# Kernel optimization log

Measured on AMD Instinct MI355X. Metric: run time of the kernel, lower is better.

## Reference

```python
import jax, jax.numpy as jnp
import numpy as np

D_MODEL = 1024
D_STATE = 16
D_CONV = 4
EXPAND = 2
D_INNER = EXPAND * D_MODEL          # 2048
DT_RANK = (D_MODEL + 15) // 16      # 64 (mamba 'auto')
B, L = 2, 1024


def _mamba_params(key, scale=0.02):
    ks = jax.random.split(key, 6)
    return dict(
        inW=jax.random.normal(ks[0], (2 * D_INNER, D_MODEL), jnp.float32) * scale,
        convW=jax.random.normal(ks[1], (D_INNER, 1, D_CONV), jnp.float32) * scale,
        convb=jnp.zeros((D_INNER,), jnp.float32),
        xprojW=jax.random.normal(ks[2], (DT_RANK + 2 * D_STATE, D_INNER), jnp.float32) * scale,
        dtW=jax.random.normal(ks[3], (D_INNER, DT_RANK), jnp.float32) * scale,
        dtb=jax.random.normal(ks[4], (D_INNER,), jnp.float32) * scale,
        A_log=jnp.log(jnp.tile(jnp.arange(1, D_STATE + 1, dtype=jnp.float32), (D_INNER, 1))),
        Dskip=jnp.ones((D_INNER,), jnp.float32),
        outW=jax.random.normal(ks[5], (D_MODEL, D_INNER), jnp.float32) * scale,
    )


def setup_inputs() -> dict:
    key = jax.random.key(0)
    kx, kf, kb, kp = jax.random.split(key, 4)
    inp = {"x": jax.random.normal(kx, (B, L, D_MODEL), jnp.float32)}
    inp["ln_w"] = jnp.ones((D_MODEL,), jnp.float32)
    inp["ln_b"] = jnp.zeros((D_MODEL,), jnp.float32)
    for pref, k in (("f_", kf), ("b_", kb)):
        for name, v in _mamba_params(k).items():
            inp[pref + name] = v
    inp["proj_W"] = jax.random.normal(kp, (D_MODEL, 2 * D_MODEL), jnp.float32) * 0.02
    inp["proj_b"] = jnp.zeros((D_MODEL,), jnp.float32)
    return inp


def _layernorm(x, w, b, eps=1e-5):
    mu = jnp.mean(x, axis=-1, keepdims=True)
    var = jnp.var(x, axis=-1, keepdims=True)
    return (x - mu) * jax.lax.rsqrt(var + eps) * w + b


def _mamba(x, inW, convW, convb, xprojW, dtW, dtb, A_log, Dskip, outW):
    # x: [B, L, d_model]
    xz = jnp.einsum('bld,ed->ble', x, inW)           # [B,L,2*d_inner]
    xs, z = jnp.split(xz, 2, axis=-1)                # each [B,L,d_inner]
    # depthwise causal conv over L
    xc = jnp.transpose(xs, (0, 2, 1))                # [B,d_inner,L]
    xc = jax.lax.conv_general_dilated(
        xc, convW, window_strides=(1,), padding=[(D_CONV - 1, 0)],
        feature_group_count=D_INNER)
    xs = jax.nn.silu(jnp.transpose(xc + convb[None, :, None], (0, 2, 1)))
    # input-dependent dt, B, C
    xdb = jnp.einsum('bld,ed->ble', xs, xprojW)      # [B,L,dt_rank+2*d_state]
    dt, Bm, Cm = jnp.split(xdb, [DT_RANK, DT_RANK + D_STATE], axis=-1)
    dt = jax.nn.softplus(jnp.einsum('blr,dr->bld', dt, dtW) + dtb)  # [B,L,d_inner]
    A = -jnp.exp(A_log)                              # [d_inner,d_state], negative
    dA = jnp.exp(dt[..., None] * A)                  # [B,L,d_inner,d_state]
    dBx = dt[..., None] * Bm[:, :, None, :] * xs[..., None]

    def step(h, inputs):
        dA_t, dBx_t, C_t = inputs                    # [B,d,s],[B,d,s],[B,s]
        h = h * dA_t + dBx_t
        y = jnp.einsum('bds,bs->bd', h, C_t)
        return h, y

    h0 = jnp.zeros((x.shape[0], D_INNER, D_STATE), x.dtype)
    _, ys = jax.lax.scan(step, h0, (jnp.moveaxis(dA, 1, 0),
                                    jnp.moveaxis(dBx, 1, 0),
                                    jnp.moveaxis(Cm, 1, 0)))
    y = jnp.moveaxis(ys, 0, 1)                       # [B,L,d_inner]
    y = (y + xs * Dskip) * jax.nn.silu(z)
    return jnp.einsum('bld,ed->ble', y, outW)        # [B,L,d_model]


def reference(x, ln_w, ln_b,
              f_inW, f_convW, f_convb, f_xprojW, f_dtW, f_dtb, f_A_log, f_Dskip, f_outW,
              b_inW, b_convW, b_convb, b_xprojW, b_dtW, b_dtb, b_A_log, b_Dskip, b_outW,
              proj_W, proj_b):
    normed = _layernorm(x, ln_w, ln_b)
    fwd_out = _mamba(normed, f_inW, f_convW, f_convb, f_xprojW, f_dtW, f_dtb,
                     f_A_log, f_Dskip, f_outW)
    bwd_out = _mamba(normed[:, ::-1, :], b_inW, b_convW, b_convb, b_xprojW, b_dtW,
                     b_dtb, b_A_log, b_Dskip, b_outW)[:, ::-1, :]
    combined = jnp.concatenate([fwd_out, bwd_out], axis=-1)
    return x + jnp.einsum('blc,ec->ble', combined, proj_W) + proj_b
```

## Files before the change

### kernel.cpp

```cpp
#include <hip/hip_runtime.h>
#include <hip/hip_bf16.h>
#include <math.h>

#define DM   1024
#define DI   2048
#define DTR  64
#define DST  16
#define NB   2
#define LL   1024
#define MR   (NB*LL)
#define XLD  128
#define KS   8

typedef __bf16 bf16x8 __attribute__((ext_vector_type(8)));
typedef float  f32x4  __attribute__((ext_vector_type(4)));

__device__ __forceinline__ float siluf(float x) { return x / (1.f + __expf(-x)); }
__device__ __forceinline__ float softplusf(float x) {
    return fmaxf(x, 0.f) + log1pf(__expf(-fabsf(x)));
}
__device__ __forceinline__ unsigned short f2bf(float f) {
    __hip_bfloat16 h = __float2bfloat16(f);
    return *reinterpret_cast<unsigned short*>(&h);
}
__device__ __forceinline__ float bf2f(__hip_bfloat16 h) { return __bfloat162float(h); }

__device__ __forceinline__ void gl2lds16(const __hip_bfloat16* g, __hip_bfloat16* l)
{
    __builtin_amdgcn_global_load_lds(
        (const __attribute__((address_space(1))) unsigned int*)g,
        (__attribute__((address_space(3))) unsigned int*)l, 16, 0, 0);
}

__global__ __launch_bounds__(256) void prep_k(
    const float* __restrict__ s0, const float* __restrict__ s1,
    const float* __restrict__ s2, const float* __restrict__ s3,
    const float* __restrict__ s4, __hip_bfloat16* __restrict__ warena,
    const float* __restrict__ fx, const float* __restrict__ bx,
    __hip_bfloat16* __restrict__ wpb2,
    const float* __restrict__ fo, const float* __restrict__ bo,
    __hip_bfloat16* __restrict__ wot,
    const float* __restrict__ x, const float* __restrict__ lnw,
    const float* __restrict__ lnb, __hip_bfloat16* __restrict__ nb)
{
    __shared__ float pshm[64 * 65];
    const int b = blockIdx.x;
    const int tid = threadIdx.x;

    if (b < 10496) {
        long idx = (long)b * 1024 + tid * 4;
        const float* src; long off;
        if      (idx <  4194304L) { src = s0; off = idx; }
        else if (idx <  8388608L) { src = s1; off = idx -  4194304L; }
        else if (idx < 10485760L) { src = s2; off = idx -  8388608L; }
        else if (idx < 10616832L) { src = s3; off = idx - 10485760L; }
        else                      { src = s4; off = idx - 10616832L; }
        float4 v = *(const float4*)(src + off);
        ushort4 o;
        o.x = f2bf(v.x); o.y = f2bf(v.y); o.z = f2bf(v.z); o.w = f2bf(v.w);
        *(ushort4*)((unsigned short*)warena + idx) = o;
    } else if (b < 10624) {
        int t = b - 10496;
        int z = t >> 6;
        const float* in = z ? bx : fx;
        int idx = ((t & 63) * 256 + tid) * 4;
        int row = idx >> 11;
        ushort4 o = make_ushort4(0, 0, 0, 0);
        if (row < 96) {
            float4 v = *(const float4*)(in + idx);
            o.x = f2bf(v.x); o.y = f2bf(v.y); o.z = f2bf(v.z); o.w = f2bf(v.w);
        }
        *(ushort4*)((unsigned short*)wpb2 + (size_t)z * 128 * DI + idx) = o;
    } else if (b < 11648) {
        int t = b - 10624;
        int z = t >> 9; t &= 511;
        const float* src = z ? bo : fo;
        int c0 = (t & 31) * 64;
        int r0 = (t >> 5) * 64;
        int tc = tid & 63;
        int tr = tid >> 6;
        #pragma unroll
        for (int ii = 0; ii < 16; ++ii) {
            int rl = tr + ii * 4;
            pshm[tc * 65 + rl] = src[(size_t)(r0 + rl) * DI + c0 + tc];
        }
        __syncthreads();
        __hip_bfloat16* dst = wot + (size_t)z * DI * DM;
        #pragma unroll
        for (int ii = 0; ii < 16; ++ii) {
            int cl = tr + ii * 4;
            dst[(size_t)(c0 + cl) * DM + r0 + tc] = __float2bfloat16(pshm[cl * 65 + tc]);
        }
    } else {
        int row = b - 11648;
        const float* xr = x + (size_t)row * DM;
        float4 v = *(const float4*)(xr + tid * 4);
        float s = v.x + v.y + v.z + v.w;
        float q = v.x*v.x + v.y*v.y + v.z*v.z + v.w*v.w;
        #pragma unroll
        for (int off = 32; off > 0; off >>= 1) {
            s += __shfl_xor(s, off, 64);
            q += __shfl_xor(q, off, 64);
        }
        int wv = tid >> 6;
        if ((tid & 63) == 0) { pshm[wv] = s; pshm[8 + wv] = q; }
        __syncthreads();
        s = pshm[0] + pshm[1] + pshm[2] + pshm[3];
        q = pshm[8] + pshm[9] + pshm[10] + pshm[11];
        float mu  = s * (1.f / DM);
        float var = q * (1.f / DM) - mu * mu;
        float rstd = rsqrtf(var + 1e-5f);
        float4 wv4 = *(const float4*)(lnw + tid * 4);
        float4 bv4 = *(const float4*)(lnb + tid * 4);
        ushort4 o;
        o.x = f2bf((v.x - mu) * rstd * wv4.x + bv4.x);
        o.y = f2bf((v.y - mu) * rstd * wv4.y + bv4.y);
        o.z = f2bf((v.z - mu) * rstd * wv4.z + bv4.z);
        o.w = f2bf((v.w - mu) * rstd * wv4.w + bv4.w);
        *(ushort4*)((unsigned short*)nb + (size_t)row * DM + tid * 4) = o;
    }
}

__global__ __launch_bounds__(256) void inproj_wcat_k(
    const __hip_bfloat16* __restrict__ nb,  const __hip_bfloat16* __restrict__ wbi,
    __hip_bfloat16* __restrict__ xz2,
    const __hip_bfloat16* __restrict__ pwb, const __hip_bfloat16* __restrict__ wot,
    __hip_bfloat16* __restrict__ wcat)
{
    __shared__ __hip_bfloat16 smem[2 * 128 * 64];
    const int z  = blockIdx.z;
    const int bxv = blockIdx.x, byv = blockIdx.y;
    if (z >= 2 && (bxv >= 16 || byv >= 8)) return;

    const __hip_bfloat16* Az;
    const __hip_bfloat16* Bz;
    __hip_bfloat16* Cz;
    int lda;
    if (z < 2) {
        Az = nb;                                lda = DM;
        Bz = wbi + (size_t)z * 2 * DI * DM;
        Cz = xz2 + (size_t)z * MR * 2 * DI;
    } else {
        Az = pwb + (size_t)(z - 2) * DM;        lda = 2 * DM;
        Bz = wot + (size_t)(z - 2) * DI * DM;
        Cz = wcat + (size_t)(z - 2) * DI;
    }
    const int ldb = DM, ldc = 2 * DI, K = DM;

    __hip_bfloat16* As = smem;
    __hip_bfloat16* Bs = smem + 128 * 64;
    const int tid  = threadIdx.x;
    const int bm   = byv * 128;
    const int bn   = bxv * 128;
    const int wv   = tid >> 6;
    const int lane = tid & 63;
    const int wr   = (wv >> 1) * 64;
    const int wc   = (wv & 1) * 64;
    const int srow = wv * 32 + (lane >> 3);
    const int cg   = ((lane & 7) ^ (lane >> 3)) * 8;
    const int fr   = lane & 15;
    const int quad = lane >> 4;
    const int pc0  = (quad ^ (fr & 7)) * 8;
    const int pc1  = ((4 + quad) ^ (fr & 7)) * 8;

    f32x4 acc[4][4] = {};

    for (int k0 = 0; k0 < K; k0 += 64) {
        __syncthreads();
        #pragma unroll
        for (int i = 0; i < 4; ++i) {
            int r = srow + i * 8;
            gl2lds16(Az + (size_t)(bm + r) * lda + k0 + cg, As + wv * 2048 + i * 512);
            gl2lds16(Bz + (size_t)(bn + r) * ldb + k0 + cg, Bs + wv * 2048 + i * 512);
        }
        __syncthreads();
        #pragma unroll
        for (int kk = 0; kk < 2; ++kk) {
            const int pc = kk ? pc1 : pc0;
            bf16x8 af[4], bf_[4];
            #pragma unroll
            for (int i = 0; i < 4; ++i) {
                af[i]  = *(const bf16x8*)(As + (wr + i * 16 + fr) * 64 + pc);
                bf_[i] = *(const bf16x8*)(Bs + (wc + i * 16 + fr) * 64 + pc);
            }
            #pragma unroll
            for (int i = 0; i < 4; ++i)
                #pragma unroll
                for (int j = 0; j < 4; ++j)
                    acc[i][j] = __builtin_amdgcn_mfma_f32_16x16x32_bf16(
                        af[i], bf_[j], acc[i][j], 0, 0, 0);
        }
    }

    float* eps = (float*)smem;
    const int half = wv >> 1;
    const int lrow = tid >> 3;
    const int cseg = (tid & 7) * 16;
    const int gr_  = bm + (lrow >> 4) * 64 + (lrow & 15);
    #pragma unroll
    for (int i = 0; i < 4; ++i) {
        __syncthreads();
        #pragma unroll
        for (int j = 0; j < 4; ++j)
            #pragma unroll
            for (int r = 0; r < 4; ++r)
                eps[(half * 16 + quad * 4 + r) * 132 + wc + j * 16 + fr] = acc[i][j][r];
        __syncthreads();
        float vals[16];
        *(float4*)(vals +  0) = *(const float4*)(eps + lrow * 132 + cseg +  0);
        *(float4*)(vals +  4) = *(const float4*)(eps + lrow * 132 + cseg +  4);
        *(float4*)(vals +  8) = *(const float4*)(eps + lrow * 132 + cseg +  8);
        *(float4*)(vals + 12) = *(const float4*)(eps + lrow * 132 + cseg + 12);
        int gr = gr_ + i * 16;
        int gc = bn + cseg;
        unsigned short os[16];
        #pragma unroll
        for (int c = 0; c < 16; ++c) os[c] = f2bf(vals[c]);
        unsigned short* dst = (unsigned short*)Cz + (size_t)gr * ldc + gc;
        *(ushort4*)(dst +  0) = *(ushort4*)(os +  0);
        *(ushort4*)(dst +  4) = *(ushort4*)(os +  4);
        *(ushort4*)(dst +  8) = *(ushort4*)(os +  8);
        *(ushort4*)(dst + 12) = *(ushort4*)(os + 12);
    }
}

template<int EPI>
__global__ __launch_bounds__(256) void gemm_gl(
    const __hip_bfloat16* __restrict__ A, int lda, size_t aofs,
    const __hip_bfloat16* __restrict__ B, int ldb, size_t bofs,
    void* __restrict__ Cp, int ldc, size_t cofs, int K,
    const float* __restrict__ bias0, const float* __restrict__ bias1)
{
    __shared__ __hip_bfloat16 smem[2 * 128 * 64];
    __hip_bfloat16* As = smem;
    __hip_bfloat16* Bs = smem + 128 * 64;
    const int tid  = threadIdx.x;
    const int z    = blockIdx.z;
    const int bm   = blockIdx.y * 128;
    const int bn   = blockIdx.x * 128;
    const __hip_bfloat16* Az = A + (size_t)z * aofs;
    const __hip_bfloat16* Bz = B + (size_t)z * bofs;
    const int wv   = tid >> 6;
    const int lane = tid & 63;
    const int wr   = (wv >> 1) * 64;
    const int wc   = (wv & 1) * 64;
    const int srow = wv * 32 + (lane >> 3);
    const int cg   = ((lane & 7) ^ (lane >> 3)) * 8;
    const int fr   = lane & 15;
    const int quad = lane >> 4;
    const int pc0  = (quad ^ (fr & 7)) * 8;
    const int pc1  = ((4 + quad) ^ (fr & 7)) * 8;

    f32x4 acc[4][4] = {};

    for (int k0 = 0; k0 < K; k0 += 64) {
        __syncthreads();
        #pragma unroll
        for (int i = 0; i < 4; ++i) {
            int r = srow + i * 8;
            gl2lds16(Az + (size_t)(bm + r) * lda + k0 + cg, As + wv * 2048 + i * 512);
            gl2lds16(Bz + (size_t)(bn + r) * ldb + k0 + cg, Bs + wv * 2048 + i * 512);
        }
        __syncthreads();
        #pragma unroll
        for (int kk = 0; kk < 2; ++kk) {
            const int pc = kk ? pc1 : pc0;
            bf16x8 af[4], bf_[4];
            #pragma unroll
            for (int i = 0; i < 4; ++i) {
                af[i]  = *(const bf16x8*)(As + (wr + i * 16 + fr) * 64 + pc);
                bf_[i] = *(const bf16x8*)(Bs + (wc + i * 16 + fr) * 64 + pc);
            }
            #pragma unroll
            for (int i = 0; i < 4; ++i)
                #pragma unroll
                for (int j = 0; j < 4; ++j)
                    acc[i][j] = __builtin_amdgcn_mfma_f32_16x16x32_bf16(
                        af[i], bf_[j], acc[i][j], 0, 0, 0);
        }
    }

    const float* bias = (EPI == 3) ? (z ? bias1 : bias0) : nullptr;
    float* eps = (float*)smem;
    const int half = wv >> 1;
    const int lrow = tid >> 3;
    const int cseg = (tid & 7) * 16;
    const int gr_  = bm + (lrow >> 4) * 64 + (lrow & 15);
    #pragma unroll
    for (int i = 0; i < 4; ++i) {
        __syncthreads();
        #pragma unroll
        for (int j = 0; j < 4; ++j)
            #pragma unroll
            for (int r = 0; r < 4; ++r)
                eps[(half * 16 + quad * 4 + r) * 132 + wc + j * 16 + fr] = acc[i][j][r];
        __syncthreads();
        float vals[16];
        *(float4*)(vals +  0) = *(const float4*)(eps + lrow * 132 + cseg +  0);
        *(float4*)(vals +  4) = *(const float4*)(eps + lrow * 132 + cseg +  4);
        *(float4*)(vals +  8) = *(const float4*)(eps + lrow * 132 + cseg +  8);
        *(float4*)(vals + 12) = *(const float4*)(eps + lrow * 132 + cseg + 12);
        int gr = gr_ + i * 16;
        int gc = bn + cseg;
        if (EPI == 0) {
            float* dst = (float*)Cp + (size_t)z * cofs + (size_t)gr * ldc + gc;
            *(float4*)(dst +  0) = *(const float4*)(vals +  0);
            *(float4*)(dst +  4) = *(const float4*)(vals +  4);
            *(float4*)(dst +  8) = *(const float4*)(vals +  8);
            *(float4*)(dst + 12) = *(const float4*)(vals + 12);
        } else {
            unsigned short os[16];
            #pragma unroll
            for (int c = 0; c < 16; ++c) {
                float t = vals[c];
                if (EPI == 3) t = softplusf(t + bias[gc + c]);
                os[c] = f2bf(t);
            }
            unsigned short* dst = (unsigned short*)Cp + (size_t)z * cofs +
                                  (size_t)gr * ldc + gc;
            *(ushort4*)(dst +  0) = *(ushort4*)(os +  0);
            *(ushort4*)(dst +  4) = *(ushort4*)(os +  4);
            *(ushort4*)(dst +  8) = *(ushort4*)(os +  8);
            *(ushort4*)(dst + 12) = *(ushort4*)(os + 12);
        }
    }
}

__global__ __launch_bounds__(256) void xproj_part_k(
    const __hip_bfloat16* __restrict__ A,
    const __hip_bfloat16* __restrict__ B,
    float* __restrict__ part)
{
    __shared__ __hip_bfloat16 smem[2 * 128 * 64];
    __hip_bfloat16* As = smem;
    __hip_bfloat16* Bs = smem + 128 * 64;
    const int tid  = threadIdx.x;
    const int ks   = blockIdx.x;
    const int bm   = blockIdx.y * 128;
    const int z    = blockIdx.z;
    const __hip_bfloat16* Az = A + (size_t)z * MR * DI;
    const __hip_bfloat16* Bz = B + (size_t)z * 128 * DI;
    const int kb   = ks * (DI / KS);
    const int wv   = tid >> 6;
    const int lane = tid & 63;
    const int wr   = (wv >> 1) * 64;
    const int wc   = (wv & 1) * 64;
    const int srow = wv * 32 + (lane >> 3);
    const int cg   = ((lane & 7) ^ (lane >> 3)) * 8;
    const int fr   = lane & 15;
    const int quad = lane >> 4;
    const int pc0  = (quad ^ (fr & 7)) * 8;
    const int pc1  = ((4 + quad) ^ (fr & 7)) * 8;

    f32x4 acc[4][4] = {};

    #pragma unroll
    for (int k0 = 0; k0 < DI / KS; k0 += 64) {
        __syncthreads();
        #pragma unroll
        for (int i = 0; i < 4; ++i) {
            int r = srow + i * 8;
            gl2lds16(Az + (size_t)(bm + r) * DI + kb + k0 + cg, As + wv * 2048 + i * 512);
            gl2lds16(Bz + (size_t)r * DI + kb + k0 + cg,        Bs + wv * 2048 + i * 512);
        }
        __syncthreads();
        #pragma unroll
        for (int kk = 0; kk < 2; ++kk) {
            const int pc = kk ? pc1 : pc0;
            bf16x8 af[4], bf_[4];
            #pragma unroll
            for (int i = 0; i < 4; ++i) {
                af[i]  = *(const bf16x8*)(As + (wr + i * 16 + fr) * 64 + pc);
                bf_[i] = *(const bf16x8*)(Bs + (wc + i * 16 + fr) * 64 + pc);
            }
            #pragma unroll
            for (int i = 0; i < 4; ++i)
                #pragma unroll
                for (int j = 0; j < 4; ++j)
                    acc[i][j] = __builtin_amdgcn_mfma_f32_16x16x32_bf16(
                        af[i], bf_[j], acc[i][j], 0, 0, 0);
        }
    }

    float* dst = part + ((size_t)z * KS + ks) * MR * XLD;
    const int er = quad * 4;
    #pragma unroll
    for (int i = 0; i < 4; ++i)
        #pragma unroll
        for (int j = 0; j < 4; ++j) {
            int row = bm + wr + i * 16 + er;
            int col = wc + j * 16 + fr;
            #pragma unroll
            for (int r = 0; r < 4; ++r)
                dst[(size_t)(row + r) * XLD + col] = acc[i][j][r];
        }
}

__global__ __launch_bounds__(256) void xproj_reduce_k(
    const float* __restrict__ part, float* __restrict__ xdb,
    __hip_bfloat16* __restrict__ xdbt)
{
    int z = blockIdx.y;
    size_t idx = ((size_t)blockIdx.x * 256 + threadIdx.x) * 4;
    const float* p = part + (size_t)z * KS * MR * XLD;
    float4 s = make_float4(0.f, 0.f, 0.f, 0.f);
    #pragma unroll
    for (int ks = 0; ks < KS; ++ks) {
        float4 v = *(const float4*)(p + (size_t)ks * MR * XLD + idx);
        s.x += v.x; s.y += v.y; s.z += v.z; s.w += v.w;
    }
    *(float4*)(xdb + (size_t)z * MR * XLD + idx) = s;
    int c = (int)(idx & (XLD - 1));
    if (c < 64) {
        size_t m = idx >> 7;
        ushort4 o;
        o.x = f2bf(s.x); o.y = f2bf(s.y); o.z = f2bf(s.z); o.w = f2bf(s.w);
        *(ushort4*)((unsigned short*)xdbt + (size_t)z * MR * 64 + m * 64 + c) = o;
    }
}

__global__ __launch_bounds__(256) void conv_silu_k(
    const __hip_bfloat16* __restrict__ xz2,
    const float* __restrict__ fW, const float* __restrict__ fb,
    const float* __restrict__ bW, const float* __restrict__ bb_,
    __hip_bfloat16* __restrict__ xsb2)
{
    int dirv = blockIdx.y;
    int idx = blockIdx.x * 256 + threadIdx.x;
    int d = idx & (DI - 1);
    int m = idx >> 11;
    int t = m & (LL - 1);
    int bb = m >> 10;
    const float* w  = (dirv ? bW : fW) + d * 4;
    const __hip_bfloat16* xz = xz2 + (size_t)dirv * MR * 2 * DI;
    float acc = (dirv ? bb_ : fb)[d];
    if (dirv == 0) {
        #pragma unroll
        for (int k = 0; k < 4; ++k) {
            int tt = t - 3 + k;
            if (tt >= 0)
                acc = fmaf(w[k], bf2f(xz[(size_t)(bb * LL + tt) * (2 * DI) + d]), acc);
        }
    } else {
        #pragma unroll
        for (int k = 0; k < 4; ++k) {
            int tt = t + 3 - k;
            if (tt < LL)
                acc = fmaf(w[k], bf2f(xz[(size_t)(bb * LL + tt) * (2 * DI) + d]), acc);
        }
    }
    xsb2[(size_t)dirv * MR * DI + (size_t)m * DI + d] = __float2bfloat16(siluf(acc));
}

__global__ __launch_bounds__(256) void scan1_k(
    const __hip_bfloat16* __restrict__ dtf2, const __hip_bfloat16* __restrict__ xsb2,
    const float* __restrict__ xdb2,
    const float* __restrict__ fA, const float* __restrict__ bA,
    float* __restrict__ hend, float* __restrict__ aprod, int G, int Cn)
{
    int d  = blockIdx.x * 256 + threadIdx.x;
    int bb = blockIdx.y;
    int zz = blockIdx.z;
    int dirv = (zz >= G) ? 1 : 0;
    int g = zz - (dirv ? G : 0);
    const float* A_log = dirv ? bA : fA;
    const __hip_bfloat16* dtf = dtf2 + (size_t)dirv * MR * DI;
    const __hip_bfloat16* xs = xsb2 + (size_t)dirv * MR * DI;
    const float* xdb = xdb2 + (size_t)dirv * MR * XLD;
    size_t hoff = (size_t)dirv * G * (NB * DI * DST);

    float Ad[DST], h[DST], ap[DST];
    bool pw = true;
    #pragma unroll
    for (int s = 0; s < DST; ++s) {
        Ad[s] = -__expf(A_log[d * DST + s]);
        pw = pw && (fabsf(Ad[s] + (float)(s + 1)) < 1e-3f * (s + 1));
        h[s] = 0.f; ap[s] = 1.f;
    }
    int i0 = g * Cn;
    for (int i = 0; i < Cn; ++i) {
        int ii = i0 + i;
        int t = dirv ? (LL - 1 - ii) : ii;
        size_t m = (size_t)bb * LL + t;
        float dtv = bf2f(dtf[m * DI + d]);
        float xv  = bf2f(xs[m * DI + d]);
        const float* bc = xdb + m * XLD;
        float dtx = dtv * xv;
        float dAv[DST];
        if (pw) {
            float r = __expf(-dtv);
            float a = r;
            #pragma unroll
            for (int s = 0; s < DST; ++s) { dAv[s] = a; a *= r; }
        } else {
            #pragma unroll
            for (int s = 0; s < DST; ++s) dAv[s] = __expf(dtv * Ad[s]);
        }
        #pragma unroll
        for (int s = 0; s < DST; ++s) {
            h[s] = fmaf(h[s], dAv[s], dtx * bc[64 + s]);
            ap[s] *= dAv[s];
        }
    }
    size_t base = hoff + ((size_t)(g * NB + bb) * DI + d) * DST;
    #pragma unroll
    for (int s = 0; s < DST; s += 4) {
        *(float4*)(hend  + base + s) = make_float4(h[s], h[s+1], h[s+2], h[s+3]);
        *(float4*)(aprod + base + s) = make_float4(ap[s], ap[s+1], ap[s+2], ap[s+3]);
    }
}

__global__ __launch_bounds__(256) void scan2_k(
    float* __restrict__ hend, const float* __restrict__ aprod, int G)
{
    int dirv = blockIdx.y;
    int idx = blockIdx.x * 256 + threadIdx.x;
    const int slab = NB * DI * DST;
    size_t hoff = (size_t)dirv * G * slab;
    float carry = 0.f;
    for (int g = 0; g < G; ++g) {
        size_t off = hoff + (size_t)g * slab + idx;
        float a = aprod[off];
        float e = hend[off];
        hend[off] = carry;
        carry = fmaf(a, carry, e);
    }
}

__global__ __launch_bounds__(256) void scan3_k(
    const __hip_bfloat16* __restrict__ dtf2, const __hip_bfloat16* __restrict__ xsb2,
    const float* __restrict__ xdb2, const __hip_bfloat16* __restrict__ xz2,
    const float* __restrict__ fA, const float* __restrict__ bA,
    const float* __restrict__ fD, const float* __restrict__ bD,
    const float* __restrict__ hin, __hip_bfloat16* __restrict__ ycat, int G, int Cn)
{
    int d  = blockIdx.x * 256 + threadIdx.x;
    int bb = blockIdx.y;
    int zz = blockIdx.z;
    int dirv = (zz >= G) ? 1 : 0;
    int g = zz - (dirv ? G : 0);
    const float* A_log = dirv ? bA : fA;
    const float* Dskip = dirv ? bD : fD;
    const __hip_bfloat16* dtf = dtf2 + (size_t)dirv * MR * DI;
    const __hip_bfloat16* xs = xsb2 + (size_t)dirv * MR * DI;
    const float* xdb = xdb2 + (size_t)dirv * MR * XLD;
    const __hip_bfloat16* xz = xz2 + (size_t)dirv * MR * 2 * DI;
    size_t hoff = (size_t)dirv * G * (NB * DI * DST);

    float Ad[DST], h[DST];
    bool pw = true;
    size_t base = hoff + ((size_t)(g * NB + bb) * DI + d) * DST;
    #pragma unroll
    for (int s = 0; s < DST; ++s) {
        Ad[s] = -__expf(A_log[d * DST + s]);
        pw = pw && (fabsf(Ad[s] + (float)(s + 1)) < 1e-3f * (s + 1));
        h[s] = hin[base + s];
    }
    float Dsk = Dskip[d];
    int i0 = g * Cn;
    for (int i = 0; i < Cn; ++i) {
        int ii = i0 + i;
        int t = dirv ? (LL - 1 - ii) : ii;
        size_t m = (size_t)bb * LL + t;
        float dtv = bf2f(dtf[m * DI + d]);
        float xv  = bf2f(xs[m * DI + d]);
        const float* bc = xdb + m * XLD;
        float dtx = dtv * xv;
        float dAv[DST];
        if (pw) {
            float r = __expf(-dtv);
            float a = r;
            #pragma unroll
            for (int s = 0; s < DST; ++s) { dAv[s] = a; a *= r; }
        } else {
            #pragma unroll
            for (int s = 0; s < DST; ++s) dAv[s] = __expf(dtv * Ad[s]);
        }
        float yv = 0.f;
        #pragma unroll
        for (int s = 0; s < DST; ++s) {
            h[s] = fmaf(h[s], dAv[s], dtx * bc[64 + s]);
            yv = fmaf(h[s], bc[80 + s], yv);
        }
        float zv = bf2f(xz[m * (2 * DI) + DI + d]);
        ycat[m * (2 * DI) + (size_t)dirv * DI + d] =
            __float2bfloat16((yv + xv * Dsk) * siluf(zv));
    }
}

__global__ __launch_bounds__(256) void scan_mono_k(
    const __hip_bfloat16* __restrict__ dtf2, const __hip_bfloat16* __restrict__ xsb2,
    const float* __restrict__ xdb2, const __hip_bfloat16* __restrict__ xz2,
    const float* __restrict__ fA, const float* __restrict__ bA,
    const float* __restrict__ fD, const float* __restrict__ bD,
    __hip_bfloat16* __restrict__ ycat)
{
    int d  = blockIdx.x * 256 + threadIdx.x;
    int bb = blockIdx.y;
    int dirv = blockIdx.z;
    const float* A_log = dirv ? bA : fA;
    const float* Dskip = dirv ? bD : fD;
    const __hip_bfloat16* dtf = dtf2 + (size_t)dirv * MR * DI;
    const __hip_bfloat16* xs = xsb2 + (size_t)dirv * MR * DI;
    const float* xdb = xdb2 + (size_t)dirv * MR * XLD;
    const __hip_bfloat16* xz = xz2 + (size_t)dirv * MR * 2 * DI;
    float Ad[DST], h[DST];
    #pragma unroll
    for (int s = 0; s < DST; ++s) { Ad[s] = -__expf(A_log[d * DST + s]); h[s] = 0.f; }
    float Dsk = Dskip[d];
    for (int i = 0; i < LL; ++i) {
        int t = dirv ? (LL - 1 - i) : i;
        size_t m = (size_t)bb * LL + t;
        float dtv = bf2f(dtf[m * DI + d]);
        float xv  = bf2f(xs[m * DI + d]);
        const float* bc = xdb + m * XLD;
        float dtx = dtv * xv;
        float yv = 0.f;
        #pragma unroll
        for (int s = 0; s < DST; ++s) {
            float dA = __expf(dtv * Ad[s]);
            h[s] = fmaf(h[s], dA, dtx * bc[64 + s]);
            yv = fmaf(h[s], bc[80 + s], yv);
        }
        float zv = bf2f(xz[m * (2 * DI) + DI + d]);
        ycat[m * (2 * DI) + (size_t)dirv * DI + d] =
            __float2bfloat16((yv + xv * Dsk) * siluf(zv));
    }
}

__global__ __launch_bounds__(256) void final_reduce_k(
    const float* __restrict__ part, const float* __restrict__ x,
    const float* __restrict__ proj_b, float* __restrict__ out)
{
    size_t idx = ((size_t)blockIdx.x * 256 + threadIdx.x) * 4;
    float4 s = make_float4(0.f, 0.f, 0.f, 0.f);
    #pragma unroll
    for (int z = 0; z < 4; ++z) {
        float4 v = *(const float4*)(part + (size_t)z * MR * DM + idx);
        s.x += v.x; s.y += v.y; s.z += v.z; s.w += v.w;
    }
    float4 xv = *(const float4*)(x + idx);
    float4 pb = *(const float4*)(proj_b + (idx & (DM - 1)));
    float4 o;
    o.x = xv.x + pb.x + s.x;
    o.y = xv.y + pb.y + s.y;
    o.z = xv.z + pb.z + s.z;
    o.w = xv.w + pb.w + s.w;
    *(float4*)(out + idx) = o;
}

extern "C" void kernel_launch(void* const* d_in, const int* in_sizes, int n_in,
                              void* d_out, int out_size, void* d_ws, size_t ws_size,
                              hipStream_t stream)
{
    const float* x      = (const float*)d_in[0];
    const float* ln_w   = (const float*)d_in[1];
    const float* ln_b   = (const float*)d_in[2];
    const float* f_inW    = (const float*)d_in[3];
    const float* f_convW  = (const float*)d_in[4];
    const float* f_convb  = (const float*)d_in[5];
    const float* f_xprojW = (const float*)d_in[6];
    const float* f_dtW    = (const float*)d_in[7];
    const float* f_dtb    = (const float*)d_in[8];
    const float* f_A_log  = (const float*)d_in[9];
    const float* f_Dskip  = (const float*)d_in[10];
    const float* f_outW   = (const float*)d_in[11];
    const float* b_inW    = (const float*)d_in[12];
    const float* b_convW  = (const float*)d_in[13];
    const float* b_convb  = (const float*)d_in[14];
    const float* b_xprojW = (const float*)d_in[15];
    const float* b_dtW    = (const float*)d_in[16];
    const float* b_dtb    = (const float*)d_in[17];
    const float* b_A_log  = (const float*)d_in[18];
    const float* b_Dskip  = (const float*)d_in[19];
    const float* b_outW   = (const float*)d_in[20];
    const float* proj_W = (const float*)d_in[21];
    const float* proj_b = (const float*)d_in[22];

    float* ws = (float*)d_ws;
    size_t o = 0;
    __hip_bfloat16* xz2  = (__hip_bfloat16*)(ws + o);
    float* fpart = ws + o;
    o += (size_t)2 * MR * 2 * DI / 2;
    __hip_bfloat16* xsb2 = (__hip_bfloat16*)(ws + o); o += (size_t)2 * MR * DI / 2;
    __hip_bfloat16* ycat = (__hip_bfloat16*)(ws + o);
    float* xpart = ws + o;
    o += (size_t)MR * 2 * DI / 2;
    float* xdb2 = ws + o; o += (size_t)2 * MR * XLD;
    __hip_bfloat16* xdbt = (__hip_bfloat16*)(ws + o); o += (size_t)2 * MR * 64 / 2;
    __hip_bfloat16* dtfb = (__hip_bfloat16*)(ws + o); o += (size_t)2 * MR * DI / 2;
    __hip_bfloat16* nb = (__hip_bfloat16*)(ws + o); o += (size_t)MR * DM / 2;
    __hip_bfloat16* warena = (__hip_bfloat16*)(ws + o); o += 15466496 / 2;
    float* hbuf = ws + o;
    size_t base_floats = o;

    __hip_bfloat16* wbi  = warena;
    __hip_bfloat16* pwb  = warena +  8388608;
    __hip_bfloat16* wdt  = warena + 10485760;
    __hip_bfloat16* wpb2 = warena + 10747904;
    __hip_bfloat16* wcat = warena + 11272192;

    const size_t slab = (size_t)NB * DI * DST;
    int G = 32;
    while (G > 4 && (base_floats + 4ull * G * slab) * 4 > ws_size) G >>= 1;
    int useChunks = ((base_floats + 4ull * G * slab) * 4 <= ws_size);
    float* hend  = hbuf;
    float* aprod = hbuf + 2ull * G * slab;
    int Cn = useChunks ? LL / G : LL;

    int wotInHbuf = useChunks && (4ull * G * slab >= 2097152ull);
    __hip_bfloat16* wot = wotInHbuf ? (__hip_bfloat16*)hbuf : xz2;

    prep_k<<<13696, 256, 0, stream>>>(
        f_inW, b_inW, proj_W, f_dtW, b_dtW, warena,
        f_xprojW, b_xprojW, wpb2,
        f_outW, b_outW, wot,
        x, ln_w, ln_b, nb);

    if (wotInHbuf) {
        inproj_wcat_k<<<dim3(32, 16, 4), 256, 0, stream>>>(
            nb, wbi, xz2, pwb, wot, wcat);
    } else {
        gemm_gl<1><<<dim3(DI / 128, DM / 128, 2), 256, 0, stream>>>(
            pwb, 2 * DM, (size_t)DM, wot, DM, (size_t)DI * DM,
            wcat, 2 * DI, (size_t)DI, DM, nullptr, nullptr);
        inproj_wcat_k<<<dim3(32, 16, 2), 256, 0, stream>>>(
            nb, wbi, xz2, pwb, wot, wcat);
    }

    conv_silu_k<<<dim3((MR * DI) / 256, 2), 256, 0, stream>>>(
        xz2, f_convW, f_convb, b_convW, b_convb, xsb2);

    xproj_part_k<<<dim3(KS, MR / 128, 2), 256, 0, stream>>>(xsb2, wpb2, xpart);
    xproj_reduce_k<<<dim3((MR * XLD) / 1024, 2), 256, 0, stream>>>(xpart, xdb2, xdbt);

    gemm_gl<3><<<dim3(DI / 128, MR / 128, 2), 256, 0, stream>>>(
        xdbt, 64, (size_t)MR * 64, wdt, 64, (size_t)DI * 64,
        dtfb, DI, (size_t)MR * DI, 64, f_dtb, b_dtb);

    if (useChunks) {
        scan1_k<<<dim3(DI / 256, NB, 2 * G), 256, 0, stream>>>(
            dtfb, xsb2, xdb2, f_A_log, b_A_log, hend, aprod, G, Cn);
        scan2_k<<<dim3((NB * DI * DST) / 256, 2), 256, 0, stream>>>(hend, aprod, G);
        scan3_k<<<dim3(DI / 256, NB, 2 * G), 256, 0, stream>>>(
            dtfb, xsb2, xdb2, xz2, f_A_log, b_A_log, f_Dskip, b_Dskip,
            hend, ycat, G, Cn);
    } else {
        scan_mono_k<<<dim3(DI / 256, NB, 2), 256, 0, stream>>>(
            dtfb, xsb2, xdb2, xz2, f_A_log, b_A_log, f_Dskip, b_Dskip, ycat);
    }

    gemm_gl<0><<<dim3(DM / 128, MR / 128, 4), 256, 0, stream>>>(
        ycat, 2 * DI, 1024, wcat, 2 * DI, 1024,
        fpart, DM, (size_t)MR * DM, 1024, nullptr, nullptr);

    final_reduce_k<<<(MR * DM) / 1024, 256, 0, stream>>>(
        fpart, x, proj_b, (float*)d_out);
}
```

Baseline: 423.2 us.

## Replace in-projection GEMM with 256x256-tile, 4-stage pipelined 512-thread kernel

The combined in-projection/wcat kernel is replaced by a dedicated in-projection GEMM that uses 256x256 output tiles with 512 threads. It streams K in 32-wide slices through a 4-deep LDS ring with explicit vmcnt waits, split barriers and MFMA priority hints. Blocks are remapped so the two directions interleave across the grid. The wcat product moves back to a separate gemm_gl launch. The larger tile raises data reuse and hides load latency, but it launches only 256 blocks, uses 128 KB of LDS per block and adds a kernel launch.

```diff
diff --git a/kernel.cpp b/kernel.cpp
--- a/kernel.cpp
+++ b/kernel.cpp
@@ -121,106 +121,117 @@
     }
 }
 
-__global__ __launch_bounds__(256) void inproj_wcat_k(
-    const __hip_bfloat16* __restrict__ nb,  const __hip_bfloat16* __restrict__ wbi,
-    __hip_bfloat16* __restrict__ xz2,
-    const __hip_bfloat16* __restrict__ pwb, const __hip_bfloat16* __restrict__ wot,
-    __hip_bfloat16* __restrict__ wcat)
-{
-    __shared__ __hip_bfloat16 smem[2 * 128 * 64];
-    const int z  = blockIdx.z;
-    const int bxv = blockIdx.x, byv = blockIdx.y;
-    if (z >= 2 && (bxv >= 16 || byv >= 8)) return;
-
-    const __hip_bfloat16* Az;
-    const __hip_bfloat16* Bz;
-    __hip_bfloat16* Cz;
-    int lda;
-    if (z < 2) {
-        Az = nb;                                lda = DM;
-        Bz = wbi + (size_t)z * 2 * DI * DM;
-        Cz = xz2 + (size_t)z * MR * 2 * DI;
-    } else {
-        Az = pwb + (size_t)(z - 2) * DM;        lda = 2 * DM;
-        Bz = wot + (size_t)(z - 2) * DI * DM;
-        Cz = wcat + (size_t)(z - 2) * DI;
-    }
-    const int ldb = DM, ldc = 2 * DI, K = DM;
-
-    __hip_bfloat16* As = smem;
-    __hip_bfloat16* Bs = smem + 128 * 64;
-    const int tid  = threadIdx.x;
-    const int bm   = byv * 128;
-    const int bn   = bxv * 128;
+__global__ __launch_bounds__(512) void inproj256_k(
+    const __hip_bfloat16* __restrict__ A,
+    const __hip_bfloat16* __restrict__ Bmat,
+    __hip_bfloat16* __restrict__ C)
+{
+    __shared__ __hip_bfloat16 smem[65536];
+    const int tid = threadIdx.x;
+    int id = blockIdx.x;
+    int s  = (id & 7) * 32 + (id >> 3);
+    const int z  = s >> 7;
+    const int r  = s & 127;
+    const int bm = (r & 7) * 256;
+    const int bn = (r >> 3) * 256;
+    const __hip_bfloat16* Az = A;
+    const __hip_bfloat16* Bz = Bmat + (size_t)z * 2 * DI * DM;
+    __hip_bfloat16* Cz = C + (size_t)z * MR * 2 * DI;
+
     const int wv   = tid >> 6;
     const int lane = tid & 63;
-    const int wr   = (wv >> 1) * 64;
-    const int wc   = (wv & 1) * 64;
-    const int srow = wv * 32 + (lane >> 3);
-    const int cg   = ((lane & 7) ^ (lane >> 3)) * 8;
+    const int wm   = wv >> 2;
+    const int wn   = wv & 3;
     const int fr   = lane & 15;
     const int quad = lane >> 4;
-    const int pc0  = (quad ^ (fr & 7)) * 8;
-    const int pc1  = ((4 + quad) ^ (fr & 7)) * 8;
-
-    f32x4 acc[4][4] = {};
-
-    for (int k0 = 0; k0 < K; k0 += 64) {
-        __syncthreads();
-        #pragma unroll
-        for (int i = 0; i < 4; ++i) {
-            int r = srow + i * 8;
-            gl2lds16(Az + (size_t)(bm + r) * lda + k0 + cg, As + wv * 2048 + i * 512);
-            gl2lds16(Bz + (size_t)(bn + r) * ldb + k0 + cg, Bs + wv * 2048 + i * 512);
-        }
-        __syncthreads();
-        #pragma unroll
-        for (int kk = 0; kk < 2; ++kk) {
-            const int pc = kk ? pc1 : pc0;
-            bf16x8 af[4], bf_[4];
-            #pragma unroll
-            for (int i = 0; i < 4; ++i) {
-                af[i]  = *(const bf16x8*)(As + (wr + i * 16 + fr) * 64 + pc);
-                bf_[i] = *(const bf16x8*)(Bs + (wc + i * 16 + fr) * 64 + pc);
-            }
-            #pragma unroll
-            for (int i = 0; i < 4; ++i)
+
+    const int r0   = tid >> 2;
+    const int ksel = ((tid & 3) ^ ((r0 >> 1) & 3)) * 8;
+    const int kph  = (quad ^ ((fr >> 1) & 3)) * 8;
+    const int aoff = (wm * 128 + fr) * 32 + kph;
+    const int boff = (wn * 64  + fr) * 32 + kph;
+
+    __hip_bfloat16* const Asl = smem;
+    __hip_bfloat16* const Bsl = smem + 32768;
+
+    f32x4 acc[8][4] = {};
+
+#define STG_A(T) { int q_ = (T) & 3; \
+    _Pragma("unroll") for (int l = 0; l < 2; ++l) \
+        gl2lds16(Az + (size_t)(bm + l * 128 + r0) * DM + (T) * 32 + ksel, \
+                 Asl + q_ * 8192 + l * 4096 + wv * 512); }
+#define STG_B(T) { int q_ = (T) & 3; \
+    _Pragma("unroll") for (int l = 0; l < 2; ++l) \
+        gl2lds16(Bz + (size_t)(bn + l * 128 + r0) * DM + (T) * 32 + ksel, \
+                 Bsl + q_ * 8192 + l * 4096 + wv * 512); }
+
+    STG_A(0); STG_B(0); STG_A(1); STG_B(1); STG_A(2); STG_B(2);
+
+#define TILE(T, VM, DOST) { \
+    asm volatile("s_barrier" ::: "memory");                \
+    if (DOST) { STG_A((T) + 3); } \
+    asm volatile("s_waitcnt vmcnt(" #VM ")" ::: "memory"); \
+    asm volatile("s_barrier" ::: "memory");                \
+    const __hip_bfloat16* At = Asl + ((T) & 3) * 8192; \
+    const __hip_bfloat16* Bt = Bsl + ((T) & 3) * 8192; \
+    bf16x8 bfr[4], afr[4]; \
+    _Pragma("unroll") for (int j = 0; j < 4; ++j) \
+        bfr[j] = *(const bf16x8*)(Bt + boff + j * 512); \
+    _Pragma("unroll") for (int i = 0; i < 4; ++i) \
+        afr[i] = *(const bf16x8*)(At + aoff + i * 512); \
+    __builtin_amdgcn_s_setprio(1); \
+    _Pragma("unroll") for (int i = 0; i < 4; ++i) \
+        _Pragma("unroll") for (int j = 0; j < 4; ++j) \
+            acc[i][j] = __builtin_amdgcn_mfma_f32_16x16x32_bf16( \
+                afr[i], bfr[j], acc[i][j], 0, 0, 0); \
+    __builtin_amdgcn_s_setprio(0); \
+    if (DOST) { STG_B((T) + 3); } \
+    asm volatile("s_barrier" ::: "memory");                \
+    _Pragma("unroll") for (int i = 0; i < 4; ++i) \
+        afr[i] = *(const bf16x8*)(At + aoff + (4 + i) * 512); \
+    __builtin_amdgcn_s_setprio(1); \
+    _Pragma("unroll") for (int i = 0; i < 4; ++i) \
+        _Pragma("unroll") for (int j = 0; j < 4; ++j) \
+            acc[4 + i][j] = __builtin_amdgcn_mfma_f32_16x16x32_bf16( \
+                afr[i], bfr[j], acc[4 + i][j], 0, 0, 0); \
+    __builtin_amdgcn_s_setprio(0); \
+}
+
+    for (int t = 0; t < 29; ++t) { TILE(t, 10, 1); }
+    TILE(29, 8, 0);
+    TILE(30, 4, 0);
+    TILE(31, 0, 0);
+#undef TILE
+#undef STG_A
+#undef STG_B
+
+    float* eps = (float*)smem;
+    const int orow = tid >> 3;
+    const int ocol = (tid & 7) * 32;
+    #pragma unroll
+    for (int p = 0; p < 4; ++p) {
+        __syncthreads();
+        if (wm == (p >> 1)) {
+            int ib = (p & 1) * 4;
+            #pragma unroll
+            for (int i2 = 0; i2 < 4; ++i2)
                 #pragma unroll
                 for (int j = 0; j < 4; ++j)
-                    acc[i][j] = __builtin_amdgcn_mfma_f32_16x16x32_bf16(
-                        af[i], bf_[j], acc[i][j], 0, 0, 0);
-        }
-    }
-
-    float* eps = (float*)smem;
-    const int half = wv >> 1;
-    const int lrow = tid >> 3;
-    const int cseg = (tid & 7) * 16;
-    const int gr_  = bm + (lrow >> 4) * 64 + (lrow & 15);
-    #pragma unroll
-    for (int i = 0; i < 4; ++i) {
-        __syncthreads();
-        #pragma unroll
-        for (int j = 0; j < 4; ++j)
-            #pragma unroll
-            for (int r = 0; r < 4; ++r)
-                eps[(half * 16 + quad * 4 + r) * 132 + wc + j * 16 + fr] = acc[i][j][r];
-        __syncthreads();
-        float vals[16];
-        *(float4*)(vals +  0) = *(const float4*)(eps + lrow * 132 + cseg +  0);
-        *(float4*)(vals +  4) = *(const float4*)(eps + lrow * 132 + cseg +  4);
-        *(float4*)(vals +  8) = *(const float4*)(eps + lrow * 132 + cseg +  8);
-        *(float4*)(vals + 12) = *(const float4*)(eps + lrow * 132 + cseg + 12);
-        int gr = gr_ + i * 16;
-        int gc = bn + cseg;
-        unsigned short os[16];
-        #pragma unroll
-        for (int c = 0; c < 16; ++c) os[c] = f2bf(vals[c]);
-        unsigned short* dst = (unsigned short*)Cz + (size_t)gr * ldc + gc;
-        *(ushort4*)(dst +  0) = *(ushort4*)(os +  0);
-        *(ushort4*)(dst +  4) = *(ushort4*)(os +  4);
-        *(ushort4*)(dst +  8) = *(ushort4*)(os +  8);
-        *(ushort4*)(dst + 12) = *(ushort4*)(os + 12);
+                    #pragma unroll
+                    for (int rr = 0; rr < 4; ++rr)
+                        eps[(i2 * 16 + quad * 4 + rr) * 260 + wn * 64 + j * 16 + fr]
+                            = acc[ib + i2][j][rr];
+        }
+        __syncthreads();
+        unsigned short os[32] __attribute__((aligned(16)));
+        #pragma unroll
+        for (int c = 0; c < 32; ++c) os[c] = f2bf(eps[orow * 260 + ocol + c]);
+        unsigned short* dst = (unsigned short*)Cz +
+            (size_t)(bm + p * 64 + orow) * (2 * DI) + bn + ocol;
+        *(uint4*)(dst +  0) = *(const uint4*)(os +  0);
+        *(uint4*)(dst +  8) = *(const uint4*)(os +  8);
+        *(uint4*)(dst + 16) = *(const uint4*)(os + 16);
+        *(uint4*)(dst + 24) = *(const uint4*)(os + 24);
     }
 }
 
@@ -718,14 +729,15 @@
         x, ln_w, ln_b, nb);
 
     if (wotInHbuf) {
-        inproj_wcat_k<<<dim3(32, 16, 4), 256, 0, stream>>>(
-            nb, wbi, xz2, pwb, wot, wcat);
+        inproj256_k<<<256, 512, 0, stream>>>(nb, wbi, xz2);
+        gemm_gl<1><<<dim3(DI / 128, DM / 128, 2), 256, 0, stream>>>(
+            pwb, 2 * DM, (size_t)DM, wot, DM, (size_t)DI * DM,
+            wcat, 2 * DI, (size_t)DI, DM, nullptr, nullptr);
     } else {
         gemm_gl<1><<<dim3(DI / 128, DM / 128, 2), 256, 0, stream>>>(
             pwb, 2 * DM, (size_t)DM, wot, DM, (size_t)DI * DM,
             wcat, 2 * DI, (size_t)DI, DM, nullptr, nullptr);
-        inproj_wcat_k<<<dim3(32, 16, 2), 256, 0, stream>>>(
-            nb, wbi, xz2, pwb, wot, wcat);
+        inproj256_k<<<256, 512, 0, stream>>>(nb, wbi, xz2);
     }
 
     conv_silu_k<<<dim3((MR * DI) / 256, 2), 256, 0, stream>>>(
```

Result: no change. 422.3 us (-0.2%).
